# Kernel tuning notes

Hardware: AMD Instinct MI355X
Metric: run time of the kernel (lower is better)

## Reference

```python
import jax, jax.numpy as jnp
import numpy as np

KSIZE = 5
# OpenCV: sigma=0 -> sigma = 0.3*((ksize-1)*0.5 - 1) + 0.8
SIGMA = 0.3 * ((KSIZE - 1) * 0.5 - 1.0) + 0.8  # = 1.1 for ksize=5


def _gauss_taps(ksize, sigma):
    r = (ksize - 1) / 2.0
    xs = np.arange(ksize, dtype=np.float64) - r
    w = np.exp(-(xs ** 2) / (2.0 * sigma ** 2))
    w /= w.sum()
    return jnp.asarray(w, dtype=jnp.float32)


def setup_inputs() -> dict:
    key = jax.random.key(0)
    x = jax.random.normal(key, (64, 384, 512, 3), dtype=jnp.float32)
    return {"x": x}


def reference(x):
    # Separable 5x5 Gaussian blur, OpenCV default border BORDER_REFLECT_101
    # (numpy/jnp 'reflect' mode, edge pixel not repeated).
    w = _gauss_taps(KSIZE, SIGMA)  # [5]
    pad = KSIZE // 2
    B, H, W, C = x.shape
    # vertical pass
    xp = jnp.pad(x, ((0, 0), (pad, pad), (0, 0), (0, 0)), mode="reflect")
    y = sum(w[k] * xp[:, k:k + H, :, :] for k in range(KSIZE))
    # horizontal pass
    yp = jnp.pad(y, ((0, 0), (0, 0), (pad, pad), (0, 0)), mode="reflect")
    out = sum(w[k] * yp[:, :, k:k + W, :] for k in range(KSIZE))
    return out
```

## Files before the change

### kernel.cpp

```cpp
#include <hip/hip_runtime.h>


#define BN 64
#define HN 384
#define WN 512
#define CN 3
#define ROWF (WN * CN)
#define ROWQ (ROWF / 4)
#define TH 4
#define DTH (2 * TH)
#define NDT (HN / DTH)
#define NTHR 512
#define NBLK (BN * NDT)

#define CW0 0.07076630f
#define CW1 0.24446040f
#define CW2 0.36954650f

typedef float vfloat4 __attribute__((ext_vector_type(4)));

__device__ __forceinline__ void vpass(const float4* win, float* vw, int l) {
#pragma unroll
    for (int r = 0; r < TH; ++r) {
        float4 a;
        a.x = CW0 * (win[r].x + win[r + 4].x) +
              CW1 * (win[r + 1].x + win[r + 3].x) + CW2 * win[r + 2].x;
        a.y = CW0 * (win[r].y + win[r + 4].y) +
              CW1 * (win[r + 1].y + win[r + 3].y) + CW2 * win[r + 2].y;
        a.z = CW0 * (win[r].z + win[r + 4].z) +
              CW1 * (win[r + 1].z + win[r + 3].z) + CW2 * win[r + 2].z;
        a.w = CW0 * (win[r].w + win[r + 4].w) +
              CW1 * (win[r + 1].w + win[r + 3].w) + CW2 * win[r + 2].w;
        ((float4*)(vw + r * 256))[l] = a;
    }
}

__device__ __forceinline__ void pads(float* vw, int q0, int l) {
    if (q0 == 0 && l < TH * 6) {
        int r = l / 6, p = l - 6 * r;
        float* vr = vw + r * 256;
        vr[2 + p] = vr[p < 3 ? 14 + p : 8 + p];
    } else if (q0 == 336 && l < TH * 6) {
        int r = l / 6, p = l - 6 * r;
        float* vr = vw + r * 256;
        vr[200 + p] = vr[p < 3 ? 194 + p : 188 + p];
    }
}

__device__ __forceinline__ void hpass(const float* vw, float* ob, int q0, int l) {
    if (l < 48) {
#pragma unroll
        for (int r = 0; r < TH; ++r) {
            const float* vr = vw + r * 256;
            float wnd[20];
#pragma unroll
            for (int k = 0; k < 5; ++k) {
                float4 t = ((const float4*)vr)[l + k];
                wnd[4 * k + 0] = t.x;
                wnd[4 * k + 1] = t.y;
                wnd[4 * k + 2] = t.z;
                wnd[4 * k + 3] = t.w;
            }
            vfloat4 res;
#pragma unroll
            for (int j = 0; j < 4; ++j) {
                res[j] =
                    CW0 * (wnd[j + 2] + wnd[j + 14]) +
                    CW1 * (wnd[j + 5] + wnd[j + 11]) +
                    CW2 * wnd[j + 8];
            }
            __builtin_nontemporal_store(res,
                &((vfloat4*)ob)[r * ROWQ + q0 + l]);
        }
    }
}

__global__ __launch_bounds__(NTHR, 6) void gauss_blur_fused(
        const float* __restrict__ x, float* __restrict__ out) {
    __shared__ float v[8 * 4 * 256];

    const int bid  = blockIdx.x;
    const int tile = (bid & 7) * (NBLK >> 3) + (bid >> 3);
    const int b    = tile / NDT;
    const int h0   = (tile - b * NDT) * DTH;
    const float* __restrict__ xb = x + (size_t)b * HN * ROWF;
    float* __restrict__ ob = out + ((size_t)b * HN + h0) * ROWF;

    const int wid = threadIdx.x >> 6;
    const int l   = threadIdx.x & 63;
    const int q0  = wid * 48;
    int c = q0 - 2 + l;
    c = c < 0 ? 0 : (c > ROWQ - 1 ? ROWQ - 1 : c);

    float4 win[12];
#pragma unroll
    for (int i = 0; i < 12; ++i) {
        int hs = h0 + i - 2;
        hs = hs < 0 ? -hs : hs;
        hs = hs >= HN ? 2 * HN - 2 - hs : hs;
        win[i] = ((const float4*)(xb + (size_t)hs * ROWF))[c];
    }
    __builtin_amdgcn_sched_barrier(0);

    float* const vw = v + wid * (TH * 256);

    vpass(win, vw, l);
    pads(vw, q0, l);
    hpass(vw, ob, q0, l);

    vpass(win + 4, vw, l);
    pads(vw, q0, l);
    hpass(vw, ob + TH * ROWF, q0, l);
}

extern "C" void kernel_launch(void* const* d_in, const int* in_sizes, int n_in,
                              void* d_out, int out_size, void* d_ws, size_t ws_size,
                              hipStream_t stream) {
    const float* x = (const float*)d_in[0];
    float* out = (float*)d_out;
    gauss_blur_fused<<<dim3(NBLK), dim3(NTHR), 0, stream>>>(x, out);
}
```

Before: 247.2 us.

## Process four row tiles per block with register-pipelined prefetch of rows

Each block now covers 16 output rows instead of 8, cycling through four 4-row tiles. It keeps a sliding register window and prefetches the next tile's input rows while the current tile is being computed. LDS staging is double-buffered per wave. This reduces the fraction of halo rows that are reloaded and lets loads overlap compute. The cost is a lower occupancy target (launch bounds 4 instead of 6), more registers, and fewer blocks in the grid.

```diff
diff --git a/kernel.cpp b/kernel.cpp
--- a/kernel.cpp
+++ b/kernel.cpp
@@ -8,7 +8,8 @@
 #define ROWF (WN * CN)
 #define ROWQ (ROWF / 4)
 #define TH 4
-#define DTH (2 * TH)
+#define NTILE 4
+#define DTH (TH * NTILE)
 #define NDT (HN / DTH)
 #define NTHR 512
 #define NBLK (BN * NDT)
@@ -75,9 +76,9 @@
     }
 }
 
-__global__ __launch_bounds__(NTHR, 6) void gauss_blur_fused(
+__global__ __launch_bounds__(NTHR, 4) void gauss_blur_fused(
         const float* __restrict__ x, float* __restrict__ out) {
-    __shared__ float v[8 * 4 * 256];
+    __shared__ float v[8 * 2 * TH * 256];
 
     const int bid  = blockIdx.x;
     const int tile = (bid & 7) * (NBLK >> 3) + (bid >> 3);
@@ -92,25 +93,52 @@
     int c = q0 - 2 + l;
     c = c < 0 ? 0 : (c > ROWQ - 1 ? ROWQ - 1 : c);
 
-    float4 win[12];
+    float4 win[8], nxt[TH];
 #pragma unroll
-    for (int i = 0; i < 12; ++i) {
+    for (int i = 0; i < 8; ++i) {
         int hs = h0 + i - 2;
         hs = hs < 0 ? -hs : hs;
-        hs = hs >= HN ? 2 * HN - 2 - hs : hs;
         win[i] = ((const float4*)(xb + (size_t)hs * ROWF))[c];
+    }
+#pragma unroll
+    for (int i = 0; i < TH; ++i) {
+        int hs = h0 + 6 + i;
+        nxt[i] = ((const float4*)(xb + (size_t)hs * ROWF))[c];
     }
     __builtin_amdgcn_sched_barrier(0);
 
-    float* const vw = v + wid * (TH * 256);
+    float* const vb = v + wid * (2 * TH * 256);
 
-    vpass(win, vw, l);
-    pads(vw, q0, l);
-    hpass(vw, ob, q0, l);
+#pragma unroll
+    for (int t = 0; t < NTILE; ++t) {
+        float4 nn[TH];
+        if (t < NTILE - 2) {
+            const int rb = h0 + 4 * t + 10;
+#pragma unroll
+            for (int i = 0; i < TH; ++i) {
+                int hs = rb + i;
+                hs = hs >= HN ? 2 * HN - 2 - hs : hs;
+                nn[i] = ((const float4*)(xb + (size_t)hs * ROWF))[c];
+            }
+            __builtin_amdgcn_sched_barrier(0);
+        }
 
-    vpass(win + 4, vw, l);
-    pads(vw, q0, l);
-    hpass(vw, ob + TH * ROWF, q0, l);
+        float* const vw = vb + (t & 1) * (TH * 256);
+        vpass(win, vw, l);
+        pads(vw, q0, l);
+        hpass(vw, ob + t * TH * ROWF, q0, l);
+
+        if (t < NTILE - 1) {
+#pragma unroll
+            for (int i = 0; i < TH; ++i) win[i] = win[i + 4];
+#pragma unroll
+            for (int i = 0; i < TH; ++i) win[TH + i] = nxt[i];
+        }
+        if (t < NTILE - 2) {
+#pragma unroll
+            for (int i = 0; i < TH; ++i) nxt[i] = nn[i];
+        }
+    }
 }
 
 extern "C" void kernel_launch(void* const* d_in, const int* in_sizes, int n_in,
```

Result: slower. 262.0 us (+6.0%).
